# Kernel optimization log

Hardware: AMD Instinct MI355X
Metric: run time of the kernel (lower is better)

## Reference

```python
import jax, jax.numpy as jnp
import numpy as np

B, N, C, H = 128, 256, 512, 2
HD = C // H  # head_dim == num_patches == N by construction of the module's einsums
ALPHA = 3.0


def _safe_pow(x, p):
    # x >= 0 (post-relu); avoid 0**p corner issues while matching x**p exactly for x>0
    pos = x > 0
    return jnp.where(pos, jnp.where(pos, x, 1.0) ** p, 0.0)


def setup_inputs() -> dict:
    key = jax.random.key(0)
    ks = jax.random.split(key, 12)
    s = 0.02
    return {
        "x": jax.random.normal(ks[0], (B, N, C), jnp.float32),
        "Wq": jax.random.normal(ks[1], (C, C), jnp.float32) * s,
        "bq": jnp.zeros((C,), jnp.float32),
        "Wk": jax.random.normal(ks[2], (C, C), jnp.float32) * s,
        "bk": jnp.zeros((C,), jnp.float32),
        "Wvs": jax.random.normal(ks[3], (C, C // 2), jnp.float32) * s,
        "bvs": jnp.zeros((C // 2,), jnp.float32),
        "Wvc": jax.random.normal(ks[4], (C, C // 2), jnp.float32) * s,
        "bvc": jnp.zeros((C // 2,), jnp.float32),
        "power": jnp.ones((1, H, 1, HD), jnp.float32),
        "W_s": jax.random.uniform(ks[5], (N, HD // 2), jnp.float32),
        "W_c": jax.random.uniform(ks[6], (N, HD // 2), jnp.float32),
        "Wp": jax.random.normal(ks[7], (C, C), jnp.float32) * s,
        "bp": jnp.zeros((C,), jnp.float32),
    }


def reference(x, Wq, bq, Wk, bk, Wvs, bvs, Wvc, bvc, power, W_s, W_c, Wp, bp):
    b, n, c = x.shape
    h, hd = H, c // H
    # projections -> [B, H, N, hd] (or hd//2 for values)
    q = (x @ Wq + bq).reshape(b, n, h, hd).transpose(0, 2, 1, 3)
    k = (x @ Wk + bk).reshape(b, n, h, hd).transpose(0, 2, 1, 3)
    v_s = (x @ Wvs + bvs).reshape(b, n, h, hd // 2).transpose(0, 2, 1, 3)
    v_c = (x @ Wvc + bvc).reshape(b, n, h, hd // 2).transpose(0, 2, 1, 3)

    power_val = 1.0 + ALPHA * jax.nn.sigmoid(power)  # [1,H,1,hd]
    q_pos = _safe_pow(jax.nn.relu(q), power_val)
    q_neg = _safe_pow(jax.nn.relu(-q), power_val)
    k_pos = _safe_pow(jax.nn.relu(k), power_val)
    k_neg = _safe_pow(jax.nn.relu(-k), power_val)

    # kv_s = einsum(k_pos,v_s)+einsum(k_neg,v_s) == einsum(k_pos+k_neg, v_s); same for kv_c
    k_abs = k_pos + k_neg
    q_abs = q_pos + q_neg
    kv_s = jnp.einsum('bhnj,bhjd->bhnd', k_abs, v_s)
    q_s_context = jnp.einsum('bhni,bhid->bhnd', q_abs, kv_s)
    kv_c = jnp.einsum('bhnj,bhjd->bhnd', k_abs, v_c)
    q_c_context = jnp.einsum('bhni,bhid->bhnd', q_abs, kv_c)

    kp_sum = k_pos.sum(-1)  # [B,H,N]
    kn_sum = k_neg.sum(-1)
    denom_s = jnp.einsum('bhni,bhi->bhn', q_pos, kp_sum) + jnp.einsum('bhni,bhi->bhn', q_neg, kn_sum)
    denom_c = jnp.einsum('bhni,bhi->bhn', q_pos, kn_sum) + jnp.einsum('bhni,bhi->bhn', q_neg, kp_sum)

    attn_s = q_s_context / (denom_s[..., None] + 1e-6) * W_s  # W_s: [N, hd//2]
    attn_c = q_c_context / (denom_c[..., None] + 1e-6) * W_c

    out = jnp.concatenate([attn_s, attn_c], axis=-1)  # [B,H,N,hd]
    out = out.transpose(0, 2, 1, 3).reshape(b, n, c)
    return out @ Wp + bp
```

## Files before the change

### kernel.cpp

```cpp
#include <hip/hip_runtime.h>
#include <hip/hip_bf16.h>
#include <math.h>

typedef unsigned int u32;
typedef short bf16x8 __attribute__((ext_vector_type(8)));
typedef float f32x4 __attribute__((ext_vector_type(4)));
typedef u32 u32x4 __attribute__((ext_vector_type(4)));

__device__ __forceinline__ float bf2f(short s) {
    u32 u = ((u32)(unsigned short)s) << 16;
    return __builtin_bit_cast(float, u);
}
__device__ __forceinline__ short f2bf(float f) {
    u32 u = __builtin_bit_cast(u32, f);
    u32 r = u + 0x7fffu + ((u >> 16) & 1u);
    return (short)(r >> 16);
}
__device__ __forceinline__ float fast_log2(float x) {
    float r; asm volatile("v_log_f32 %0, %1" : "=v"(r) : "v"(x)); return r;
}
__device__ __forceinline__ float fast_exp2(float x) {
    float r; asm volatile("v_exp_f32 %0, %1" : "=v"(r) : "v"(x)); return r;
}
__device__ __forceinline__ void gload_lds16(const short* g, short* lds) {
    __builtin_amdgcn_global_load_lds(
        (const __attribute__((address_space(1))) u32*)g,
        (__attribute__((address_space(3))) u32*)lds, 16, 0, 0);
}
__device__ __forceinline__ bf16x8 stripsign(bf16x8 v) {
    u32x4 u = __builtin_bit_cast(u32x4, v);
    u &= 0x7fff7fffu;
    return __builtin_bit_cast(bf16x8, u);
}

struct P {
    const float* bcat; const float* pcol;
    short* qa; short* ka;
    short* vt; short* kvt;
    const float* dsb; const float* dcb; const float* Ws; const float* Wc;
    short* Y; float* out;
};

__global__ void k_pack(const float* __restrict__ Wq, const float* __restrict__ Wk,
                       const float* __restrict__ Wvs, const float* __restrict__ Wvc,
                       const float* __restrict__ Wp,
                       const float* __restrict__ bq, const float* __restrict__ bk,
                       const float* __restrict__ bvs, const float* __restrict__ bvc,
                       const float* __restrict__ bp, const float* __restrict__ power,
                       short* __restrict__ WcatT, float* __restrict__ bcat, float* __restrict__ pcol)
{
    int i = blockIdx.x * 256 + threadIdx.x;
    int r = i >> 9, k = i & 511;
    int rs = r;
    if (r < 1024 || r >= 1536)
        rs = (r & ~63) | ((r & 15) << 2) | ((r >> 4) & 3);
    float w;
    if (rs < 512)       w = Wq[k * 512 + rs];
    else if (rs < 1024) w = Wk[k * 512 + (rs - 512)];
    else if (rs < 1536) {
        int rr = rs - 1024; int h = rr >> 8; int d = rr & 255;
        w = (d < 128) ? Wvs[k * 256 + h * 128 + d] : Wvc[k * 256 + h * 128 + (d - 128)];
    } else             w = Wp[k * 512 + (rs - 1536)];
    WcatT[i] = f2bf(w);

    if (i < 2048) {
        float bb;
        if (i < 512)       bb = bq[i];
        else if (i < 1024) bb = bk[i - 512];
        else if (i < 1536) {
            int rr = i - 1024; int h = rr >> 8; int d = rr & 255;
            bb = (d < 128) ? bvs[h * 128 + d] : bvc[h * 128 + (d - 128)];
        } else             bb = bp[i - 1536];
        bcat[i] = bb;
    }
    if (i < 512) pcol[i] = 1.0f + 3.0f / (1.0f + expf(-power[i]));
}

__global__ void k_cast(const float* __restrict__ x, short* __restrict__ xb)
{
    int i = blockIdx.x * 256 + threadIdx.x;
    float4 v = ((const float4*)x)[i];
    short4 s;
    s.x = f2bf(v.x); s.y = f2bf(v.y); s.z = f2bf(v.z); s.w = f2bf(v.w);
    ((short4*)xb)[i] = s;
}

__global__ void k_ksum(const short* __restrict__ ka,
                       float* __restrict__ kpsum, float* __restrict__ knsum)
{
    int gid = blockIdx.x * 256 + threadIdx.x;
    int gw = gid >> 6;
    int lane = gid & 63;
    short4 a4 = ((const short4*)(ka + ((size_t)gw << 8)))[lane];
    short aa[4] = {a4.x, a4.y, a4.z, a4.w};
    float sp = 0.f, sn = 0.f;
#pragma unroll
    for (int j = 0; j < 4; ++j) {
        float a = fabsf(bf2f(aa[j]));
        if (((unsigned short)aa[j] >> 15) == 0) sp += a; else sn += a;
    }
#pragma unroll
    for (int m = 1; m < 64; m <<= 1) { sp += __shfl_xor(sp, m, 64); sn += __shfl_xor(sn, m, 64); }
    if (lane == 0) { kpsum[gw] = sp; knsum[gw] = sn; }
}

__global__ void k_denom(const short* __restrict__ qa,
                        const float* __restrict__ kpsum, const float* __restrict__ knsum,
                        float* __restrict__ dsb, float* __restrict__ dcb)
{
    int gid = blockIdx.x * 256 + threadIdx.x;
    int gw = gid >> 6;
    int lane = gid & 63;
    int bhl = gw >> 8;
    short4 q4 = ((const short4*)(qa + ((size_t)gw << 8)))[lane];
    float4 kp4 = ((const float4*)(kpsum + ((size_t)bhl << 8)))[lane];
    float4 kn4 = ((const float4*)(knsum + ((size_t)bhl << 8)))[lane];
    short qq[4] = {q4.x, q4.y, q4.z, q4.w};
    float kp[4] = {kp4.x, kp4.y, kp4.z, kp4.w};
    float kn[4] = {kn4.x, kn4.y, kn4.z, kn4.w};
    float ss = 0.f, sc = 0.f;
#pragma unroll
    for (int j = 0; j < 4; ++j) {
        float a = fabsf(bf2f(qq[j]));
        if (((unsigned short)qq[j] >> 15) == 0) { ss += a * kp[j]; sc += a * kn[j]; }
        else                                    { ss += a * kn[j]; sc += a * kp[j]; }
    }
#pragma unroll
    for (int m = 1; m < 64; m <<= 1) { ss += __shfl_xor(ss, m, 64); sc += __shfl_xor(sc, m, 64); }
    if (lane == 0) { dsb[gw] = ss; dcb[gw] = sc; }
}

#define MODE_QK  0
#define MODE_VT  1
#define MODE_KV  2
#define MODE_CTX 3
#define MODE_OUT 4

template <int MODE>
__launch_bounds__(256, 4)
__global__ void gemm_nt(const short* __restrict__ Ag, const short* __restrict__ Bg,
                        int K, int tilesN, P p)
{
    __shared__ short As[128 * 64];
    __shared__ short Bs[128 * 64];

    const int nwg = gridDim.x * gridDim.y;
    const int s = blockIdx.y * gridDim.x + blockIdx.x;
    const int cpx = nwg >> 3;
    const int lin = (s & 7) * cpx + (s >> 3);

    int tm, tn, bhl;
    if (MODE == MODE_KV || MODE == MODE_CTX) {
        bhl = lin >> 2;
        int rem = lin & 3;
        tm = rem / tilesN; tn = rem % tilesN;
    } else {
        bhl = 0;
        tm = lin / tilesN; tn = lin % tilesN;
    }

    const short* A = Ag;
    const short* B = Bg;
    if (MODE == MODE_KV || MODE == MODE_CTX) {
        A += (size_t)bhl << 16;
        B += (size_t)bhl << 16;
    }
    constexpr bool stripA = (MODE == MODE_CTX);
    constexpr bool stripB = (MODE == MODE_KV);

    const int t = threadIdx.x;
    const int lane = t & 63;
    const int w = t >> 6;
    const int wr = w >> 1, wc = w & 1;

    f32x4 acc[4][4];
#pragma unroll
    for (int i = 0; i < 4; ++i)
#pragma unroll
        for (int j = 0; j < 4; ++j) acc[i][j] = 0.f;

    const int nkt = K >> 6;
    for (int kt = 0; kt < nkt; ++kt) {
#pragma unroll
        for (int q4i = 0; q4i < 4; ++q4i) {
            int seg = w * 4 + q4i;
            int r = seg * 8 + (lane >> 3);
            int c = (lane & 7) ^ (r & 7);
            gload_lds16(A + (size_t)(tm * 128 + r) * K + kt * 64 + c * 8, &As[seg * 512]);
            gload_lds16(B + (size_t)(tn * 128 + r) * K + kt * 64 + c * 8, &Bs[seg * 512]);
        }
        __syncthreads();
#pragma unroll
        for (int kk = 0; kk < 2; ++kk) {
            bf16x8 af[4], bfr[4];
#pragma unroll
            for (int mt = 0; mt < 4; ++mt) {
                int row = wr * 64 + mt * 16 + (lane & 15);
                int ch = kk * 4 + (lane >> 4);
                af[mt] = *(const bf16x8*)(&As[row * 64 + ((ch ^ (row & 7)) << 3)]);
                if constexpr (stripA) af[mt] = stripsign(af[mt]);
            }
#pragma unroll
            for (int nt = 0; nt < 4; ++nt) {
                int row = wc * 64 + nt * 16 + (lane & 15);
                int ch = kk * 4 + (lane >> 4);
                bfr[nt] = *(const bf16x8*)(&Bs[row * 64 + ((ch ^ (row & 7)) << 3)]);
                if constexpr (stripB) bfr[nt] = stripsign(bfr[nt]);
            }
#pragma unroll
            for (int mt = 0; mt < 4; ++mt)
#pragma unroll
                for (int nt = 0; nt < 4; ++nt)
                    acc[mt][nt] = __builtin_amdgcn_mfma_f32_16x16x32_bf16(af[mt], bfr[nt], acc[mt][nt], 0, 0, 0);
        }
        __syncthreads();
    }

    if (MODE == MODE_QK) {
#pragma unroll
        for (int mt = 0; mt < 4; ++mt) {
#pragma unroll
            for (int r = 0; r < 4; ++r) {
                int n_g = tm * 128 + wr * 64 + mt * 16 + (lane >> 4) * 4 + r;
                int l0  = tn * 128 + wc * 64 + (lane & 15) * 4;
                short4 sv;
#pragma unroll
                for (int nt = 0; nt < 4; ++nt) {
                    int lg = l0 + nt;
                    float v = acc[mt][nt][r] + p.bcat[lg];
                    float pw = p.pcol[lg & 511];
                    float a = (v != 0.0f) ? fast_exp2(pw * fast_log2(fabsf(v))) : 0.0f;
                    unsigned short sa = (unsigned short)f2bf(a);
                    sa |= (unsigned short)((__builtin_bit_cast(u32, v) >> 16) & 0x8000u);
                    ((short*)&sv)[nt] = (short)sa;
                }
                int bl = n_g >> 8, n = n_g & 255;
                int h = (l0 >> 8) & 1;
                short* dst = (l0 < 512) ? p.qa : p.ka;
                *(short4*)(dst + (((size_t)((bl * 2 + h) * 256 + n)) << 8) + (l0 & 255)) = sv;
            }
        }
    } else if (MODE == MODE_VT) {
#pragma unroll
        for (int mt = 0; mt < 4; ++mt) {
#pragma unroll
            for (int nt = 0; nt < 4; ++nt) {
                int d_g = tn * 128 + wc * 64 + nt * 16 + (lane & 15);
                int n0  = tm * 128 + wr * 64 + mt * 16 + (lane >> 4) * 4;
                float bias = p.bcat[1024 + d_g];
                short4 sv;
#pragma unroll
                for (int r = 0; r < 4; ++r)
                    ((short*)&sv)[r] = f2bf(acc[mt][nt][r] + bias);
                int bl = n0 >> 8;
                int h = d_g >> 8, d = d_g & 255;
                *(short4*)(p.vt + (((size_t)((bl * 2 + h) * 256 + d)) << 8) + (n0 & 255)) = sv;
            }
        }
    } else if (MODE == MODE_OUT) {
#pragma unroll
        for (int mt = 0; mt < 4; ++mt) {
#pragma unroll
            for (int r = 0; r < 4; ++r) {
                int row_g = tm * 128 + wr * 64 + mt * 16 + (lane >> 4) * 4 + r;
                int l0 = tn * 128 + wc * 64 + (lane & 15) * 4;
                float4 fv;
#pragma unroll
                for (int nt = 0; nt < 4; ++nt)
                    ((float*)&fv)[nt] = acc[mt][nt][r] + p.bcat[1536 + l0 + nt];
                *(float4*)(p.out + ((size_t)row_g << 9) + l0) = fv;
            }
        }
    } else {
#pragma unroll
        for (int mt = 0; mt < 4; ++mt) {
#pragma unroll
            for (int nt = 0; nt < 4; ++nt) {
#pragma unroll
                for (int r = 0; r < 4; ++r) {
                    int row = tm * 128 + wr * 64 + mt * 16 + (lane >> 4) * 4 + r;
                    int col = tn * 128 + wc * 64 + nt * 16 + (lane & 15);
                    float v = acc[mt][nt][r];
                    if (MODE == MODE_KV) {
                        p.kvt[((size_t)bhl << 16) + (row << 8) + col] = f2bf(v);
                    } else {
                        int n = row, d = col;
                        float den = ((d < 128) ? p.dsb : p.dcb)[bhl * 256 + n] + 1e-6f;
                        float wgt = (d < 128) ? p.Ws[n * 128 + d] : p.Wc[n * 128 + (d - 128)];
                        v = v / den * wgt;
                        int bl = bhl >> 1, h = bhl & 1;
                        p.Y[((size_t)(bl * 256 + n) << 9) + h * 256 + d] = f2bf(v);
                    }
                }
            }
        }
    }
}

extern "C" void kernel_launch(void* const* d_in, const int* in_sizes, int n_in,
                              void* d_out, int out_size, void* d_ws, size_t ws_size,
                              hipStream_t stream)
{
    const float* x     = (const float*)d_in[0];
    const float* Wq    = (const float*)d_in[1];
    const float* bq    = (const float*)d_in[2];
    const float* Wk    = (const float*)d_in[3];
    const float* bk    = (const float*)d_in[4];
    const float* Wvs   = (const float*)d_in[5];
    const float* bvs   = (const float*)d_in[6];
    const float* Wvc   = (const float*)d_in[7];
    const float* bvc   = (const float*)d_in[8];
    const float* power = (const float*)d_in[9];
    const float* Ws    = (const float*)d_in[10];
    const float* Wc    = (const float*)d_in[11];
    const float* Wp    = (const float*)d_in[12];
    const float* bp    = (const float*)d_in[13];
    (void)in_sizes; (void)n_in; (void)out_size; (void)ws_size;

    char* ws = (char*)d_ws;
    size_t off = 0;
    auto alloc = [&](size_t bytes) { void* pp = ws + off; off += (bytes + 255) & ~(size_t)255; return pp; };
    short* Wcat = (short*)alloc(2097152);
    float* bcat = (float*)alloc(8192);
    float* pcol = (float*)alloc(2048);
    short* xb   = (short*)alloc(33554432);
    short* qa   = (short*)alloc(33554432);
    short* ka   = (short*)alloc(33554432);
    short* vt   = (short*)alloc(33554432);
    short* kvt  = (short*)alloc(33554432);
    float* kpsum= (float*)alloc(262144);
    float* knsum= (float*)alloc(262144);
    float* dsb  = (float*)alloc(262144);
    float* dcb  = (float*)alloc(262144);

    P p{};
    p.bcat = bcat; p.pcol = pcol;
    p.qa = qa; p.ka = ka;
    p.vt = vt; p.kvt = kvt;
    p.dsb = dsb; p.dcb = dcb; p.Ws = Ws; p.Wc = Wc;
    p.Y = xb; p.out = nullptr;

    k_pack<<<4096, 256, 0, stream>>>(Wq, Wk, Wvs, Wvc, Wp, bq, bk, bvs, bvc, bp, power, Wcat, bcat, pcol);

    k_cast<<<16384, 256, 0, stream>>>(x, xb);

    gemm_nt<MODE_QK><<<dim3(2048, 1), 256, 0, stream>>>(xb, Wcat, 512, 8, p);

    gemm_nt<MODE_VT><<<dim3(1024, 1), 256, 0, stream>>>(xb, Wcat + 1024 * 512, 512, 4, p);

    gemm_nt<MODE_KV><<<dim3(4, 256), 256, 0, stream>>>(vt, ka, 256, 2, p);

    k_ksum<<<16384, 256, 0, stream>>>(ka, kpsum, knsum);
    k_denom<<<16384, 256, 0, stream>>>(qa, kpsum, knsum, dsb, dcb);

    gemm_nt<MODE_CTX><<<dim3(4, 256), 256, 0, stream>>>(qa, kvt, 256, 2, p);

    P po = p;
    po.out = (float*)d_out;
    gemm_nt<MODE_OUT><<<dim3(1024, 1), 256, 0, stream>>>(xb, Wcat + 1536 * 512, 512, 4, po);
}
```

Before: 237.7 us.

## Stage GEMM epilogues through LDS for coalesced 16-byte global stores

```diff
diff --git a/kernel.cpp b/kernel.cpp
--- a/kernel.cpp
+++ b/kernel.cpp
@@ -51,16 +51,13 @@
 {
     int i = blockIdx.x * 256 + threadIdx.x;
     int r = i >> 9, k = i & 511;
-    int rs = r;
-    if (r < 1024 || r >= 1536)
-        rs = (r & ~63) | ((r & 15) << 2) | ((r >> 4) & 3);
     float w;
-    if (rs < 512)       w = Wq[k * 512 + rs];
-    else if (rs < 1024) w = Wk[k * 512 + (rs - 512)];
-    else if (rs < 1536) {
-        int rr = rs - 1024; int h = rr >> 8; int d = rr & 255;
+    if (r < 512)       w = Wq[k * 512 + r];
+    else if (r < 1024) w = Wk[k * 512 + (r - 512)];
+    else if (r < 1536) {
+        int rr = r - 1024; int h = rr >> 8; int d = rr & 255;
         w = (d < 128) ? Wvs[k * 256 + h * 128 + d] : Wvc[k * 256 + h * 128 + (d - 128)];
-    } else             w = Wp[k * 512 + (rs - 1536)];
+    } else             w = Wp[k * 512 + (r - 1536)];
     WcatT[i] = f2bf(w);
 
     if (i < 2048) {
@@ -141,8 +138,9 @@
 __global__ void gemm_nt(const short* __restrict__ Ag, const short* __restrict__ Bg,
                         int K, int tilesN, P p)
 {
-    __shared__ short As[128 * 64];
-    __shared__ short Bs[128 * 64];
+    __shared__ __align__(16) short sm[16384];
+    short* As = sm;
+    short* Bs = sm + 8192;
 
     const int nwg = gridDim.x * gridDim.y;
     const int s = blockIdx.y * gridDim.x + blockIdx.x;
@@ -216,60 +214,87 @@
         __syncthreads();
     }
 
-    if (MODE == MODE_QK) {
+    if (MODE == MODE_QK || MODE == MODE_VT) {
 #pragma unroll
         for (int mt = 0; mt < 4; ++mt) {
 #pragma unroll
-            for (int r = 0; r < 4; ++r) {
-                int n_g = tm * 128 + wr * 64 + mt * 16 + (lane >> 4) * 4 + r;
-                int l0  = tn * 128 + wc * 64 + (lane & 15) * 4;
-                short4 sv;
-#pragma unroll
-                for (int nt = 0; nt < 4; ++nt) {
-                    int lg = l0 + nt;
-                    float v = acc[mt][nt][r] + p.bcat[lg];
-                    float pw = p.pcol[lg & 511];
-                    float a = (v != 0.0f) ? fast_exp2(pw * fast_log2(fabsf(v))) : 0.0f;
-                    unsigned short sa = (unsigned short)f2bf(a);
-                    sa |= (unsigned short)((__builtin_bit_cast(u32, v) >> 16) & 0x8000u);
-                    ((short*)&sv)[nt] = (short)sa;
+            for (int nt = 0; nt < 4; ++nt) {
+#pragma unroll
+                for (int r = 0; r < 4; ++r) {
+                    int lrow = wr * 64 + mt * 16 + (lane >> 4) * 4 + r;
+                    int lcol = wc * 64 + nt * 16 + (lane & 15);
+                    float v = acc[mt][nt][r];
+                    short sv;
+                    if (MODE == MODE_QK) {
+                        int col_g = tn * 128 + lcol;
+                        v += p.bcat[col_g];
+                        float pw = p.pcol[col_g & 511];
+                        float a = (v != 0.0f) ? fast_exp2(pw * fast_log2(fabsf(v))) : 0.0f;
+                        unsigned short sa = (unsigned short)f2bf(a);
+                        sa |= (unsigned short)((__builtin_bit_cast(u32, v) >> 16) & 0x8000u);
+                        sv = (short)sa;
+                    } else {
+                        v += p.bcat[1024 + tm * 128 + lrow];
+                        sv = f2bf(v);
+                    }
+                    int g = lcol >> 3;
+                    sm[lrow * 128 + ((g ^ (lrow & 7)) << 3) + (lcol & 7)] = sv;
                 }
-                int bl = n_g >> 8, n = n_g & 255;
-                int h = (l0 >> 8) & 1;
-                short* dst = (l0 < 512) ? p.qa : p.ka;
-                *(short4*)(dst + (((size_t)((bl * 2 + h) * 256 + n)) << 8) + (l0 & 255)) = sv;
-            }
-        }
-    } else if (MODE == MODE_VT) {
-#pragma unroll
-        for (int mt = 0; mt < 4; ++mt) {
-#pragma unroll
-            for (int nt = 0; nt < 4; ++nt) {
-                int d_g = tn * 128 + wc * 64 + nt * 16 + (lane & 15);
-                int n0  = tm * 128 + wr * 64 + mt * 16 + (lane >> 4) * 4;
-                float bias = p.bcat[1024 + d_g];
-                short4 sv;
-#pragma unroll
-                for (int r = 0; r < 4; ++r)
-                    ((short*)&sv)[r] = f2bf(acc[mt][nt][r] + bias);
-                int bl = n0 >> 8;
+            }
+        }
+        __syncthreads();
+#pragma unroll
+        for (int i = 0; i < 8; ++i) {
+            int slot = i * 256 + t;
+            int lrow = slot >> 4;
+            int g = slot & 15;
+            bf16x8 val = *(const bf16x8*)&sm[lrow * 128 + ((g ^ (lrow & 7)) << 3)];
+            if (MODE == MODE_QK) {
+                int row_g = tm * 128 + lrow;
+                int col0 = tn * 128 + g * 8;
+                int bl = row_g >> 8, n = row_g & 255;
+                int h = (col0 >> 8) & 1;
+                short* dst = (col0 < 512) ? p.qa : p.ka;
+                *(bf16x8*)(dst + (((size_t)((bl * 2 + h) * 256 + n)) << 8) + (col0 & 255)) = val;
+            } else {
+                int d_g = tm * 128 + lrow;
+                int col0 = tn * 128 + g * 8;
                 int h = d_g >> 8, d = d_g & 255;
-                *(short4*)(p.vt + (((size_t)((bl * 2 + h) * 256 + d)) << 8) + (n0 & 255)) = sv;
+                int bl = col0 >> 8, n0 = col0 & 255;
+                *(bf16x8*)(p.vt + (((size_t)((bl * 2 + h) * 256 + d)) << 8) + n0) = val;
             }
         }
     } else if (MODE == MODE_OUT) {
-#pragma unroll
-        for (int mt = 0; mt < 4; ++mt) {
-#pragma unroll
-            for (int r = 0; r < 4; ++r) {
-                int row_g = tm * 128 + wr * 64 + mt * 16 + (lane >> 4) * 4 + r;
-                int l0 = tn * 128 + wc * 64 + (lane & 15) * 4;
-                float4 fv;
-#pragma unroll
-                for (int nt = 0; nt < 4; ++nt)
-                    ((float*)&fv)[nt] = acc[mt][nt][r] + p.bcat[1536 + l0 + nt];
-                *(float4*)(p.out + ((size_t)row_g << 9) + l0) = fv;
-            }
+        float* smf = (float*)sm;
+#pragma unroll
+        for (int half = 0; half < 2; ++half) {
+            if (wr == half) {
+#pragma unroll
+                for (int mt = 0; mt < 4; ++mt) {
+#pragma unroll
+                    for (int nt = 0; nt < 4; ++nt) {
+#pragma unroll
+                        for (int r = 0; r < 4; ++r) {
+                            int lrow = mt * 16 + (lane >> 4) * 4 + r;
+                            int lcol = wc * 64 + nt * 16 + (lane & 15);
+                            float v = acc[mt][nt][r] + p.bcat[1536 + tn * 128 + lcol];
+                            int g = lcol >> 2;
+                            smf[lrow * 128 + ((g ^ (lrow & 7)) << 2) + (lcol & 3)] = v;
+                        }
+                    }
+                }
+            }
+            __syncthreads();
+#pragma unroll
+            for (int i = 0; i < 8; ++i) {
+                int slot = i * 256 + t;
+                int lrow = slot >> 5;
+                int g = slot & 31;
+                float4 val = *(const float4*)&smf[lrow * 128 + ((g ^ (lrow & 7)) << 2)];
+                int row_g = tm * 128 + half * 64 + lrow;
+                *(float4*)(p.out + ((size_t)row_g << 9) + tn * 128 + g * 4) = val;
+            }
+            __syncthreads();
         }
     } else {
 #pragma unroll
@@ -346,7 +371,7 @@
 
     gemm_nt<MODE_QK><<<dim3(2048, 1), 256, 0, stream>>>(xb, Wcat, 512, 8, p);
 
-    gemm_nt<MODE_VT><<<dim3(1024, 1), 256, 0, stream>>>(xb, Wcat + 1024 * 512, 512, 4, p);
+    gemm_nt<MODE_VT><<<dim3(1024, 1), 256, 0, stream>>>(Wcat + 1024 * 512, xb, 512, 256, p);
 
     gemm_nt<MODE_KV><<<dim3(4, 256), 256, 0, stream>>>(vt, ka, 256, 2, p);
 
```

Result: faster. 207.3 us (-12.8%).
